# Kernel tuning notes

Hardware: AMD Instinct MI355X
Metric: run time of the kernel (lower is better)

Reference implementation:

```python
import jax, jax.numpy as jnp
import numpy as np

B, S, D = 2, 2048, 1024
H = 16
KEY_DIM = 1024   # full projected dim; original scales by sqrt(key_dim), NOT head_dim
VAL_DIM = 1024
OUT_DIM = 1024


def setup_inputs() -> dict:
    key = jax.random.key(0)
    ks = jax.random.split(key, 11)
    s = 0.02
    return {
        "queries": jax.random.normal(ks[0], (B, S, D), jnp.float32),
        "keys": jax.random.normal(ks[1], (B, S, D), jnp.float32),
        "values": jax.random.normal(ks[2], (B, S, D), jnp.float32),
        "Wq": jax.random.normal(ks[3], (D, KEY_DIM), jnp.float32) * s,
        "bq": jnp.zeros((KEY_DIM,), jnp.float32),
        "Wk": jax.random.normal(ks[4], (D, KEY_DIM), jnp.float32) * s,
        "bk": jnp.zeros((KEY_DIM,), jnp.float32),
        "Wv": jax.random.normal(ks[5], (D, VAL_DIM), jnp.float32) * s,
        "bv": jnp.zeros((VAL_DIM,), jnp.float32),
        "Wo": jax.random.normal(ks[6], (KEY_DIM, OUT_DIM), jnp.float32) * s,
        "bo": jnp.zeros((OUT_DIM,), jnp.float32),
    }


def _split_heads(x):
    # [B, S, H*dh] -> [B, H, S, dh]
    b, s, _ = x.shape
    return x.reshape(b, s, H, -1).transpose(0, 2, 1, 3)


def reference(queries, keys, values, Wq, bq, Wk, bk, Wv, bv, Wo, bo):
    q = _split_heads(queries @ Wq + bq)   # [B,H,S,dk]
    k = _split_heads(keys @ Wk + bk)      # [B,H,S,dk]
    v = _split_heads(values @ Wv + bv)    # [B,H,S,dv]
    scale = jnp.sqrt(jnp.float32(KEY_DIM))  # full key_dim, as in the source
    scores = jnp.einsum('bhqd,bhkd->bhqk', q, k) / scale  # [B,H,S,S]
    # Source calls F.softmax with no dim; torch's legacy rule picks dim=1
    # (the heads axis) for a 4-D tensor. Reproduced faithfully.
    weights = jax.nn.softmax(scores, axis=1)
    o = jnp.einsum('bhqk,bhkd->bhqd', weights, v)          # [B,H,S,dv]
    o = o.transpose(0, 2, 1, 3).reshape(B, S, KEY_DIM)     # merge heads
    return o @ Wo + bo
```

## Files before the change

### kernel.cpp

```cpp
#include <hip/hip_runtime.h>


typedef unsigned short ushort;
typedef __attribute__((ext_vector_type(8))) short short8;
typedef __attribute__((ext_vector_type(4))) short short4v;
typedef __attribute__((ext_vector_type(4))) float f32x4;
typedef __attribute__((ext_vector_type(4))) float float4v;
typedef __attribute__((ext_vector_type(4))) unsigned int uint4v;
typedef __attribute__((ext_vector_type(2))) unsigned int uint2v;

#define MFMA32(a, b, c) __builtin_amdgcn_mfma_f32_16x16x32_bf16(a, b, c, 0, 0, 0)
#define MFMA16(a, b, c) __builtin_amdgcn_mfma_f32_16x16x16bf16_1k(a, b, c, 0, 0, 0)

#define VMCNT(N) asm volatile("s_waitcnt vmcnt(" #N ")" ::: "memory")
#define SCHEDBAR() __builtin_amdgcn_sched_barrier(0)
#define BARRIER() __builtin_amdgcn_s_barrier()

__device__ __forceinline__ ushort f2bf(float f) {
    unsigned u = __float_as_uint(f);
    u += 0x7fffu + ((u >> 16) & 1u);
    return (ushort)(u >> 16);
}
__device__ __forceinline__ ushort f2hf(float f) {
    union { _Float16 h; ushort u; } c;
    c.h = (_Float16)f;
    return c.u;
}
__device__ __forceinline__ float hf2f(ushort h) {
    union { ushort u; _Float16 h; } c;
    c.u = h;
    return (float)c.h;
}

__device__ __forceinline__ void gload16(const ushort* g, ushort* l) {
    __builtin_amdgcn_global_load_lds(
        (__attribute__((address_space(1))) void*)(unsigned long long)(g),
        (__attribute__((address_space(3))) void*)(l), 16, 0, 0);
}

__global__ __launch_bounds__(256) void convert_x_kernel(
    const float* __restrict__ q, const float* __restrict__ k,
    const float* __restrict__ v, ushort* __restrict__ out) {
    const size_t NPER = 4194304ull;
    size_t idx = ((size_t)blockIdx.x * 256 + threadIdx.x) * 8;
    const size_t stride = (size_t)gridDim.x * 256 * 8;
    for (; idx < 3 * NPER; idx += stride) {
        const float* src;
        size_t off;
        if (idx < NPER)          { src = q; off = idx; }
        else if (idx < 2 * NPER) { src = k; off = idx - NPER; }
        else                     { src = v; off = idx - 2 * NPER; }
        float4v a = *(const float4v*)(src + off);
        float4v b = *(const float4v*)(src + off + 4);
        union { ushort u[8]; uint4v v4; } pk;
        #pragma unroll
        for (int j = 0; j < 4; j++) { pk.u[j] = f2bf(a[j]); pk.u[4 + j] = f2bf(b[j]); }
        *(uint4v*)(out + idx) = pk.v4;
    }
}

__global__ __launch_bounds__(256) void transpose_w_kernel(
    const float* __restrict__ w0, const float* __restrict__ w1,
    const float* __restrict__ w2, const float* __restrict__ w3,
    ushort* __restrict__ Wt) {
    const float* W = blockIdx.z == 0 ? w0 : blockIdx.z == 1 ? w1 : blockIdx.z == 2 ? w2 : w3;
    ushort* out = Wt + (size_t)blockIdx.z * 1024 * 1024;
    __shared__ ushort st[64 * 72];
    int t = threadIdx.x;
    int kb = blockIdx.y * 64, nb = blockIdx.x * 64;
    int c4 = (t & 15) * 4;
    int r0 = t >> 4;
    #pragma unroll
    for (int p = 0; p < 4; p++) {
        int r = r0 + p * 16;
        float4v f = *(const float4v*)(W + (size_t)(kb + r) * 1024 + nb + c4);
        union { ushort u[4]; uint2v v2; } pk;
        #pragma unroll
        for (int j = 0; j < 4; j++) pk.u[j] = f2bf(f[j]);
        *(uint2v*)(st + r * 72 + c4) = pk.v2;
    }
    __syncthreads();
    int n = t >> 2;
    int kc = (t & 3) * 16;
    union { ushort u[16]; uint4v v4[2]; } tw;
    #pragma unroll
    for (int j = 0; j < 16; j++) tw.u[j] = st[(kc + j) * 72 + n];
    uint4v* dst = (uint4v*)(out + (size_t)(nb + n) * 1024 + kb + kc);
    dst[0] = tw.v4[0];
    dst[1] = tw.v4[1];
}

__device__ __forceinline__ void gemm_core(
    const ushort* __restrict__ A, const ushort* __restrict__ Bt,
    const float* __restrict__ bias, ushort* __restrict__ Cb,
    float* __restrict__ Cf, int mode, ushort* sA, ushort* sB) {
    int tid = threadIdx.x, lane = tid & 63, wave = tid >> 6;
    int li = lane & 15, g = lane >> 4;
    int mt = blockIdx.y * 128, nt = blockIdx.x * 128;
    int wm = (wave >> 1) * 64, wn = (wave & 1) * 64;
    f32x4 acc[4][4] = {};
    for (int k0 = 0; k0 < 1024; k0 += 64) {
        __syncthreads();
        #pragma unroll
        for (int i = 0; i < 4; i++) {
            int c = tid + i * 256;
            int row = c >> 3, chd = c & 7;
            int cg = chd ^ (row & 7);
            gload16(A + (size_t)(mt + row) * 1024 + k0 + cg * 8, sA + c * 8);
            gload16(Bt + (size_t)(nt + row) * 1024 + k0 + cg * 8, sB + c * 8);
        }
        __syncthreads();
        #pragma unroll
        for (int kk = 0; kk < 2; kk++) {
            short8 af[4], bfr[4];
            #pragma unroll
            for (int i = 0; i < 4; i++) {
                int ra = wm + i * 16 + li;
                int cb = kk * 64 + g * 16;
                af[i] = *(const short8*)((char*)sA + ra * 128 + (cb ^ ((ra & 7) << 4)));
                int rb = wn + i * 16 + li;
                bfr[i] = *(const short8*)((char*)sB + rb * 128 + (cb ^ ((rb & 7) << 4)));
            }
            #pragma unroll
            for (int mi = 0; mi < 4; mi++)
                #pragma unroll
                for (int ni = 0; ni < 4; ni++)
                    acc[mi][ni] = MFMA32(af[mi], bfr[ni], acc[mi][ni]);
        }
    }
    #pragma unroll
    for (int mi = 0; mi < 4; mi++) {
        #pragma unroll
        for (int ni = 0; ni < 4; ni++) {
            int n = nt + wn + ni * 16 + li;
            int m0 = mt + wm + mi * 16 + g * 4;
            float bv = bias[n];
            if (mode == 0) {
                #pragma unroll
                for (int r = 0; r < 4; r++)
                    Cb[(size_t)(m0 + r) * 1024 + n] = f2bf(acc[mi][ni][r] + bv);
            } else if (mode == 1) {
                int batch = m0 >> 11, mm = m0 & 2047;
                union { ushort u[4]; uint2v v2; } pk;
                #pragma unroll
                for (int r = 0; r < 4; r++) pk.u[r] = f2bf(acc[mi][ni][r] + bv);
                *(uint2v*)(Cb + (size_t)batch * 1024 * 2048 + (size_t)n * 2048 + mm) = pk.v2;
            } else {
                #pragma unroll
                for (int r = 0; r < 4; r++)
                    Cf[(size_t)(m0 + r) * 1024 + n] = acc[mi][ni][r] + bv;
            }
        }
    }
}

__global__ __launch_bounds__(256, 2) void proj_kernel(
    const ushort* __restrict__ Xb, const ushort* __restrict__ Wt,
    const float* __restrict__ bq, const float* __restrict__ bk,
    const float* __restrict__ bv, ushort* __restrict__ Qb,
    ushort* __restrict__ Kb, ushort* __restrict__ Vtb) {
    __shared__ ushort sA[128 * 64];
    __shared__ ushort sB[128 * 64];
    int z = blockIdx.z;
    const float* bias = z == 0 ? bq : (z == 1 ? bk : bv);
    ushort* out = z == 0 ? Qb : (z == 1 ? Kb : Vtb);
    gemm_core(Xb + (size_t)z * 4194304ull, Wt + (size_t)z * 1048576ull,
              bias, out, nullptr, z == 2 ? 1 : 0, sA, sB);
}

__global__ __launch_bounds__(256, 2) void outproj_kernel(
    const ushort* __restrict__ Ob, const ushort* __restrict__ Wt3,
    const float* __restrict__ bo, float* __restrict__ out) {
    __shared__ ushort sA[128 * 64];
    __shared__ ushort sB[128 * 64];
    gemm_core(Ob, Wt3, bo, nullptr, out, 2, sA, sB);
}

__global__ __launch_bounds__(256, 2) void zsum_kernel(
    const ushort* __restrict__ Qb, const ushort* __restrict__ Kb,
    ushort* __restrict__ Zln) {
    __shared__ ushort sQ[64 * 64];
    __shared__ ushort sK[128 * 64];
    int tid = threadIdx.x, lane = tid & 63, wid = tid >> 6;
    int li = lane & 15, g = lane >> 4;
    int bid = blockIdx.x;
    int swz = (bid & 7) * 128 + (bid >> 3);
    int qt = swz & 31, C = swz >> 5;
    int b = C >> 4, kg = C & 15;
    int q0 = qt * 64, k0 = kg * 128;
    const ushort* Qp = Qb + (size_t)(b * 2048 + q0) * 1024;
    const ushort* Kp = Kb + (size_t)(b * 2048 + k0) * 1024;
    f32x4 zacc[4][2] = {};
    for (int h = 0; h < 16; h++) {
        int co = h * 64;
        __syncthreads();
        #pragma unroll
        for (int i = 0; i < 2; i++) {
            int c = tid + i * 256;
            int r = c >> 3, m = c & 7;
            gload16(Qp + (size_t)r * 1024 + co + (m ^ (r & 7)) * 8, sQ + c * 8);
        }
        #pragma unroll
        for (int i = 0; i < 4; i++) {
            int c = tid + i * 256;
            int r = c >> 3, m = c & 7;
            gload16(Kp + (size_t)r * 1024 + co + (m ^ (r & 7)) * 8, sK + c * 8);
        }
        __syncthreads();
        short8 qf[4][2], kf[2][2];
        #pragma unroll
        for (int qs = 0; qs < 4; qs++)
            #pragma unroll
            for (int dc = 0; dc < 2; dc++) {
                int row = qs * 16 + li;
                qf[qs][dc] = *(const short8*)(
                    (char*)sQ + row * 128 + ((dc * 64 + g * 16) ^ ((row & 7) << 4)));
            }
        #pragma unroll
        for (int ks = 0; ks < 2; ks++)
            #pragma unroll
            for (int dc = 0; dc < 2; dc++) {
                int row = wid * 32 + ks * 16 + li;
                kf[ks][dc] = *(const short8*)(
                    (char*)sK + row * 128 + ((dc * 64 + g * 16) ^ ((row & 7) << 4)));
            }
        #pragma unroll
        for (int qs = 0; qs < 4; qs++)
            #pragma unroll
            for (int ks = 0; ks < 2; ks++) {
                f32x4 st = {0.f, 0.f, 0.f, 0.f};
                st = MFMA32(kf[ks][0], qf[qs][0], st);
                st = MFMA32(kf[ks][1], qf[qs][1], st);
                #pragma unroll
                for (int r = 0; r < 4; r++)
                    zacc[qs][ks][r] += __expf(st[r] * 0.03125f);
            }
    }
    #pragma unroll
    for (int qs = 0; qs < 4; qs++)
        #pragma unroll
        for (int ks = 0; ks < 2; ks++) {
            union { ushort u[4]; uint2v v; } pk;
            #pragma unroll
            for (int r = 0; r < 4; r++)
                pk.u[r] = f2hf(__logf(zacc[qs][ks][r]));
            *(uint2v*)(Zln + (size_t)(b * 2048 + q0 + qs * 16 + li) * 2048 +
                       k0 + wid * 32 + ks * 16 + g * 4) = pk.v;
        }
}

__global__ __launch_bounds__(256, 2) void pv_kernel(
    const ushort* __restrict__ Qb, const ushort* __restrict__ Kb,
    const ushort* __restrict__ Vt, const ushort* __restrict__ Zln,
    ushort* __restrict__ Ob) {
    __shared__ ushort sK[2][4 * 32 * 64];
    __shared__ ushort sV[2][4 * 64 * 32];
    __shared__ ushort sZ[2][32 * 32];
    int tid = threadIdx.x, lane = tid & 63, hh = tid >> 6;
    int li = lane & 15, g = lane >> 4;
    int bid = blockIdx.x;
    int swz = (bid & 7) * 64 + (bid >> 3);
    int hp = swz & 3, p = swz >> 2;
    int b = p >> 6, qt = p & 63;
    int q0 = qt * 32;
    int head = hp * 4 + hh;
    short8 qf[2][2];
    #pragma unroll
    for (int qs = 0; qs < 2; qs++)
        #pragma unroll
        for (int dc = 0; dc < 2; dc++)
            qf[qs][dc] = *(const short8*)(
                Qb + (size_t)(b * 2048 + q0 + qs * 16 + li) * 1024 +
                head * 64 + dc * 32 + g * 8);
    f32x4 oacc[2][4] = {};
    int kc_r = (tid >> 3) & 31, kc_m = tid & 7;
    int vc_r = (tid >> 2) & 63, vc_m = tid & 3;
    int zc_r = (tid & 127) >> 2, zc_m = tid & 3;
    const ushort* Kst = Kb + (size_t)(b * 2048 + kc_r) * 1024 + hp * 256 +
                        (kc_m ^ (kc_r & 7)) * 8;
    const ushort* Vst = Vt + (size_t)(b * 1024 + hp * 256 + vc_r) * 2048 +
                        (vc_m ^ ((vc_r >> 1) & 3)) * 8;
    const ushort* Zst = Zln + (size_t)(b * 2048 + q0 + zc_r) * 2048 +
                        (zc_m ^ ((zc_r >> 1) & 3)) * 8;
    #define PV_STAGE(BUF, KB)                                                  \
        {                                                                      \
            _Pragma("unroll") for (int i = 0; i < 4; i++)                      \
                gload16(Kst + (size_t)(KB) * 1024 + i * 64,                    \
                        sK[BUF] + (tid + i * 256) * 8);                        \
            _Pragma("unroll") for (int i = 0; i < 4; i++)                      \
                gload16(Vst + (size_t)i * 64 * 2048 + (KB),                    \
                        sV[BUF] + (tid + i * 256) * 8);                        \
            if (tid < 128) gload16(Zst + (KB), sZ[BUF] + tid * 8);             \
        }
    PV_STAGE(0, 0)
    for (int it = 0; it < 64; ++it) {
        int cur = it & 1;
        int kb = it * 32;
        if (it + 1 < 64) {
            PV_STAGE(cur ^ 1, kb + 32)
            if (hh < 2) { VMCNT(9); } else { VMCNT(8); }
        } else {
            VMCNT(0);
        }
        SCHEDBAR();
        BARRIER();
        short8 kf[2][2];
        #pragma unroll
        for (int ks = 0; ks < 2; ks++)
            #pragma unroll
            for (int dc = 0; dc < 2; dc++) {
                int rk = ks * 16 + li;
                kf[ks][dc] = *(const short8*)(
                    (char*)sK[cur] + hh * 4096 + rk * 128 +
                    ((dc * 64 + g * 16) ^ ((rk & 7) << 4)));
            }
        short4v pf[2][2];
        #pragma unroll
        for (int qs = 0; qs < 2; qs++)
            #pragma unroll
            for (int ks = 0; ks < 2; ks++) {
                f32x4 st = {0.f, 0.f, 0.f, 0.f};
                st = MFMA32(kf[ks][0], qf[qs][0], st);
                st = MFMA32(kf[ks][1], qf[qs][1], st);
                int sl = ks * 4 + g;
                int rq = qs * 16 + li;
                union { ushort u[4]; uint2v v; } rz;
                rz.v = *(const uint2v*)(
                    (char*)sZ[cur] + rq * 64 +
                    (((sl >> 1) ^ ((rq >> 1) & 3)) * 2 + (sl & 1)) * 8);
                float e0 = __expf(__builtin_fmaf(st[0], 0.03125f, -hf2f(rz.u[0])));
                float e1 = __expf(__builtin_fmaf(st[1], 0.03125f, -hf2f(rz.u[1])));
                float e2 = __expf(__builtin_fmaf(st[2], 0.03125f, -hf2f(rz.u[2])));
                float e3 = __expf(__builtin_fmaf(st[3], 0.03125f, -hf2f(rz.u[3])));
                unsigned a0 = __float_as_uint(e0) + 0x8000u;
                unsigned a1 = __float_as_uint(e1) + 0x8000u;
                unsigned a2 = __float_as_uint(e2) + 0x8000u;
                unsigned a3 = __float_as_uint(e3) + 0x8000u;
                union { unsigned u[2]; short4v s; } pk;
                pk.u[0] = __builtin_amdgcn_perm(a1, a0, 0x07060302u);
                pk.u[1] = __builtin_amdgcn_perm(a3, a2, 0x07060302u);
                pf[qs][ks] = pk.s;
            }
        #pragma unroll
        for (int ks = 0; ks < 2; ks++) {
            int sl = ks * 4 + g;
            #pragma unroll
            for (int ds = 0; ds < 4; ds++) {
                int rv = ds * 16 + li;
                short4v vf = *(const short4v*)(
                    (char*)sV[cur] + hh * 4096 + rv * 64 +
                    (((sl >> 1) ^ ((rv >> 1) & 3)) * 2 + (sl & 1)) * 8);
                oacc[0][ds] = MFMA16(pf[0][ks], vf, oacc[0][ds]);
                oacc[1][ds] = MFMA16(pf[1][ks], vf, oacc[1][ds]);
            }
        }
        BARRIER();
    }
    #undef PV_STAGE
    ushort* Oo = Ob + (size_t)(b * 2048 + q0) * 1024 + head * 64;
    #pragma unroll
    for (int qs = 0; qs < 2; qs++)
        #pragma unroll
        for (int ds = 0; ds < 4; ds++)
            #pragma unroll
            for (int r = 0; r < 4; r++)
                Oo[(size_t)(qs * 16 + g * 4 + r) * 1024 + ds * 16 + li] =
                    f2bf(oacc[qs][ds][r]);
}

extern "C" void kernel_launch(void* const* d_in, const int* in_sizes, int n_in,
                              void* d_out, int out_size, void* d_ws, size_t ws_size,
                              hipStream_t stream) {
    const float* queries = (const float*)d_in[0];
    const float* keys    = (const float*)d_in[1];
    const float* values  = (const float*)d_in[2];
    const float* Wq = (const float*)d_in[3];
    const float* bq = (const float*)d_in[4];
    const float* Wk = (const float*)d_in[5];
    const float* bk = (const float*)d_in[6];
    const float* Wv = (const float*)d_in[7];
    const float* bv = (const float*)d_in[8];
    const float* Wo = (const float*)d_in[9];
    const float* bo = (const float*)d_in[10];
    float* out = (float*)d_out;

    ushort* Xb  = (ushort*)d_ws;
    ushort* Wt  = Xb + 12ull * 1024 * 1024;
    ushort* Qb  = Wt + 4ull * 1024 * 1024;
    ushort* Kb  = Qb + 4ull * 1024 * 1024;
    ushort* Vtb = Kb + 4ull * 1024 * 1024;
    ushort* Zln = Xb;
    ushort* Ob  = Xb + 8ull * 1024 * 1024;

    convert_x_kernel<<<2048, 256, 0, stream>>>(queries, keys, values, Xb);
    transpose_w_kernel<<<dim3(16, 16, 4), 256, 0, stream>>>(Wq, Wk, Wv, Wo, Wt);
    proj_kernel<<<dim3(8, 32, 3), 256, 0, stream>>>(Xb, Wt, bq, bk, bv, Qb, Kb, Vtb);
    zsum_kernel<<<1024, 256, 0, stream>>>(Qb, Kb, Zln);
    pv_kernel<<<512, 256, 0, stream>>>(Qb, Kb, Vtb, Zln, Ob);
    outproj_kernel<<<dim3(8, 32), 256, 0, stream>>>(Ob, Wt + 3ull * 1024 * 1024, bo, out);
}
```

Before: 188.1 us.

## Give each wave private LDS staging buffers and drop block barriers in PV loop

The PV kernel's shared K/V/Z staging, which all four waves filled cooperatively, is replaced by per-wave double-buffered LDS regions. Each wave now loads only its own head's K and V slice plus its own copy of the Z tile. Each wave then waits only on its own vmcnt, so both s_barrier calls per iteration go away and waves no longer stall on each other. The cost is that the Z tile is fetched four times per block, and LDS use grows to about 80 KB per block, which may strain the two-blocks-per-CU occupancy target.

```diff
diff --git a/kernel.cpp b/kernel.cpp
--- a/kernel.cpp
+++ b/kernel.cpp
@@ -14,7 +14,6 @@
 
 #define VMCNT(N) asm volatile("s_waitcnt vmcnt(" #N ")" ::: "memory")
 #define SCHEDBAR() __builtin_amdgcn_sched_barrier(0)
-#define BARRIER() __builtin_amdgcn_s_barrier()
 
 __device__ __forceinline__ ushort f2bf(float f) {
     unsigned u = __float_as_uint(f);
@@ -253,17 +252,15 @@
     const ushort* __restrict__ Qb, const ushort* __restrict__ Kb,
     const ushort* __restrict__ Vt, const ushort* __restrict__ Zln,
     ushort* __restrict__ Ob) {
-    __shared__ ushort sK[2][4 * 32 * 64];
-    __shared__ ushort sV[2][4 * 64 * 32];
-    __shared__ ushort sZ[2][32 * 32];
-    int tid = threadIdx.x, lane = tid & 63, hh = tid >> 6;
+    __shared__ ushort S[4][2][5120];
+    int tid = threadIdx.x, lane = tid & 63, wv = tid >> 6;
     int li = lane & 15, g = lane >> 4;
     int bid = blockIdx.x;
     int swz = (bid & 7) * 64 + (bid >> 3);
     int hp = swz & 3, p = swz >> 2;
     int b = p >> 6, qt = p & 63;
     int q0 = qt * 32;
-    int head = hp * 4 + hh;
+    int head = hp * 4 + wv;
     short8 qf[2][2];
     #pragma unroll
     for (int qs = 0; qs < 2; qs++)
@@ -273,24 +270,32 @@
                 Qb + (size_t)(b * 2048 + q0 + qs * 16 + li) * 1024 +
                 head * 64 + dc * 32 + g * 8);
     f32x4 oacc[2][4] = {};
-    int kc_r = (tid >> 3) & 31, kc_m = tid & 7;
-    int vc_r = (tid >> 2) & 63, vc_m = tid & 3;
-    int zc_r = (tid & 127) >> 2, zc_m = tid & 3;
-    const ushort* Kst = Kb + (size_t)(b * 2048 + kc_r) * 1024 + hp * 256 +
-                        (kc_m ^ (kc_r & 7)) * 8;
-    const ushort* Vst = Vt + (size_t)(b * 1024 + hp * 256 + vc_r) * 2048 +
-                        (vc_m ^ ((vc_r >> 1) & 3)) * 8;
-    const ushort* Zst = Zln + (size_t)(b * 2048 + q0 + zc_r) * 2048 +
-                        (zc_m ^ ((zc_r >> 1) & 3)) * 8;
+    const ushort* Ksrc[4];
+    const ushort* Vsrc[4];
+    const ushort* Zsrc[2];
+    #pragma unroll
+    for (int i = 0; i < 4; i++) {
+        int c = lane + i * 64;
+        int kr = c >> 3, km = c & 7;
+        Ksrc[i] = Kb + (size_t)(b * 2048 + kr) * 1024 + head * 64 + (km ^ (kr & 7)) * 8;
+        int vr = c >> 2, vm = c & 3;
+        Vsrc[i] = Vt + (size_t)(b * 1024 + head * 64 + vr) * 2048 + (vm ^ ((vr >> 1) & 3)) * 8;
+    }
+    #pragma unroll
+    for (int i = 0; i < 2; i++) {
+        int c = lane + i * 64;
+        int zr = c >> 2, zm = c & 3;
+        Zsrc[i] = Zln + (size_t)(b * 2048 + q0 + zr) * 2048 + (zm ^ ((zr >> 1) & 3)) * 8;
+    }
     #define PV_STAGE(BUF, KB)                                                  \
         {                                                                      \
+            ushort* dst = S[wv][BUF];                                          \
             _Pragma("unroll") for (int i = 0; i < 4; i++)                      \
-                gload16(Kst + (size_t)(KB) * 1024 + i * 64,                    \
-                        sK[BUF] + (tid + i * 256) * 8);                        \
+                gload16(Ksrc[i] + (size_t)(KB) * 1024, dst + (lane + i * 64) * 8); \
             _Pragma("unroll") for (int i = 0; i < 4; i++)                      \
-                gload16(Vst + (size_t)i * 64 * 2048 + (KB),                    \
-                        sV[BUF] + (tid + i * 256) * 8);                        \
-            if (tid < 128) gload16(Zst + (KB), sZ[BUF] + tid * 8);             \
+                gload16(Vsrc[i] + (KB), dst + 2048 + (lane + i * 64) * 8);     \
+            _Pragma("unroll") for (int i = 0; i < 2; i++)                      \
+                gload16(Zsrc[i] + (KB), dst + 4096 + (lane + i * 64) * 8);     \
         }
     PV_STAGE(0, 0)
     for (int it = 0; it < 64; ++it) {
@@ -298,12 +303,12 @@
         int kb = it * 32;
         if (it + 1 < 64) {
             PV_STAGE(cur ^ 1, kb + 32)
-            if (hh < 2) { VMCNT(9); } else { VMCNT(8); }
+            VMCNT(10);
         } else {
             VMCNT(0);
         }
         SCHEDBAR();
-        BARRIER();
+        const char* Wb = (const char*)S[wv][cur];
         short8 kf[2][2];
         #pragma unroll
         for (int ks = 0; ks < 2; ks++)
@@ -311,8 +316,7 @@
             for (int dc = 0; dc < 2; dc++) {
                 int rk = ks * 16 + li;
                 kf[ks][dc] = *(const short8*)(
-                    (char*)sK[cur] + hh * 4096 + rk * 128 +
-                    ((dc * 64 + g * 16) ^ ((rk & 7) << 4)));
+                    Wb + rk * 128 + ((dc * 64 + g * 16) ^ ((rk & 7) << 4)));
             }
         short4v pf[2][2];
         #pragma unroll
@@ -326,7 +330,7 @@
                 int rq = qs * 16 + li;
                 union { ushort u[4]; uint2v v; } rz;
                 rz.v = *(const uint2v*)(
-                    (char*)sZ[cur] + rq * 64 +
+                    Wb + 8192 + rq * 64 +
                     (((sl >> 1) ^ ((rq >> 1) & 3)) * 2 + (sl & 1)) * 8);
                 float e0 = __expf(__builtin_fmaf(st[0], 0.03125f, -hf2f(rz.u[0])));
                 float e1 = __expf(__builtin_fmaf(st[1], 0.03125f, -hf2f(rz.u[1])));
@@ -348,13 +352,12 @@
             for (int ds = 0; ds < 4; ds++) {
                 int rv = ds * 16 + li;
                 short4v vf = *(const short4v*)(
-                    (char*)sV[cur] + hh * 4096 + rv * 64 +
+                    Wb + 4096 + rv * 64 +
                     (((sl >> 1) ^ ((rv >> 1) & 3)) * 2 + (sl & 1)) * 8);
                 oacc[0][ds] = MFMA16(pf[0][ks], vf, oacc[0][ds]);
                 oacc[1][ds] = MFMA16(pf[1][ks], vf, oacc[1][ds]);
             }
         }
-        BARRIER();
     }
     #undef PV_STAGE
     ushort* Oo = Ob + (size_t)(b * 2048 + q0) * 1024 + head * 64;
```

After: 181.7 us. 3.4% less time.
